# Optimization experiments

Hardware: AMD Instinct MI355X
Metric: run time of the kernel (lower is better)

Reference implementation:

```python
import jax, jax.numpy as jnp
import numpy as np


def _conv2d(x, w, b, dilation=1):
    pad = dilation * (w.shape[-1] // 2)
    y = jax.lax.conv_general_dilated(x, w, (1, 1), [(pad, pad), (pad, pad)],
                                     rhs_dilation=(dilation, dilation),
                                     dimension_numbers=("NCHW", "OIHW", "NCHW"))
    return y + b[None, :, None, None]


def _bn(x, gamma, beta, mean, var):
    # eval-mode BatchNorm2d, eps=1e-5
    inv = gamma / jnp.sqrt(var + 1e-5)
    return (x - mean[None, :, None, None]) * inv[None, :, None, None] + beta[None, :, None, None]


def _frft2d(x, angles):
    # Faithful port of the source frft2d, including the quirk that
    # temp[shft, :] indexes the BATCH dim: since shft is a permutation of
    # 0..N-1, the net effect is that batch entries 0..N-1 get (i)fft'd along
    # axis -2 and entries >= N are untouched.
    temp = jnp.swapaxes(x, -1, -2)
    BC = temp.shape[0]
    for a in angles:
        a = a % 4
        N = temp.shape[-2]
        sN = np.float32(np.sqrt(N))
        mask = (jnp.arange(BC) < N)[:, None, None]
        if a == 1:
            temp = jnp.where(mask, jnp.fft.fft(temp, axis=-2) / sN, temp)
        elif a == 2:
            temp = jnp.flip(temp, axis=-2)
        elif a == 3:
            temp = jnp.where(mask, jnp.fft.ifft(temp, axis=-2) * sN, temp)
        temp = jnp.swapaxes(temp, -1, -2)
    return temp


def setup_inputs() -> dict:
    key = jax.random.key(0)
    ks = jax.random.split(key, 12)
    B, C, H, W = 4, 64, 256, 256
    f = lambda k, shape, s=0.1: jax.random.normal(k, shape, dtype=jnp.float32) * s
    z1 = jnp.zeros((1,), jnp.float32)
    o1 = jnp.ones((1,), jnp.float32)
    return {
        "x": jax.random.normal(ks[0], (B, C, H, W), dtype=jnp.float32),
        "kernel_map": jnp.ones((H, W), dtype=jnp.float32),
        "theta_w": f(ks[1], (1, 1, 3, 3)), "theta_b": z1,
        "phase_w": f(ks[2], (1, 1, 3, 3)), "phase_b": z1,
        "phase_gamma": o1, "phase_beta": z1, "phase_mean": z1, "phase_var": o1,
        "amp_w": f(ks[3], (1, 1, 1, 1)), "amp_b": z1,
        "ms_w1": f(ks[4], (1, 1, 3, 3)), "ms_b1": z1,
        "ms_w2": f(ks[5], (1, 1, 3, 3)), "ms_b2": z1,
        "ms_w3": f(ks[6], (1, 1, 3, 3)), "ms_b3": z1,
        "fc1_w": f(ks[7], (16, 1)), "fc1_b": jnp.zeros((16,), jnp.float32),
        "fc2_w": f(ks[8], (1, 16)), "fc2_b": z1,
        "fin_w": f(ks[9], (1, 6, 1, 1)), "fin_b": z1,
        "fin_gamma": o1, "fin_beta": z1, "fin_mean": z1, "fin_var": o1,
    }


def reference(x, kernel_map, theta_w, theta_b, phase_w, phase_b,
              phase_gamma, phase_beta, phase_mean, phase_var,
              amp_w, amp_b, ms_w1, ms_b1, ms_w2, ms_b2, ms_w3, ms_b3,
              fc1_w, fc1_b, fc2_w, fc2_b, fin_w, fin_b,
              fin_gamma, fin_beta, fin_mean, fin_var):
    B, C, H, W = x.shape
    BC = B * C
    xf = x.reshape(BC, H, W)
    trker = jnp.clip(jax.nn.softplus(kernel_map), 1e-3, 10.0)
    # Riesz kernels, p=(1,1) => sin(pi/2)
    Y = (jnp.arange(H, dtype=jnp.float32) + 1.0)[:, None]
    X = (jnp.arange(W, dtype=jnp.float32) + 1.0)[None, :]
    sa = np.float32(np.sin(0.5 * np.pi))
    denom = jnp.sqrt((X / sa) ** 2 + (Y / sa) ** 2) + 1e-6
    dx = ((-1j) * (X / sa) / denom).astype(jnp.complex64) * trker
    dy = ((-1j) * (Y / sa) / denom).astype(jnp.complex64) * trker
    fa = _frft2d(xf.astype(jnp.complex64), [1, 1])
    R1 = jnp.abs(_frft2d(dx * fa, [-1, -1])) + 1e-6
    R2 = jnp.abs(_frft2d(dy * fa, [-1, -1])) + 1e-6
    A = jnp.sqrt(jax.nn.relu(xf ** 2 + R1 ** 2 + R2 ** 2) + 1e-6)[:, None]
    P = jnp.arctan2(jnp.sqrt(R1 ** 2 + R2 ** 2) + 1e-6, xf + 1e-6)[:, None]
    theta = jnp.arctan2(R2, R1 + 1e-6)[:, None]
    G_theta = theta * jax.nn.sigmoid(_conv2d(theta, theta_w, theta_b))
    P_prime = jax.nn.relu(_bn(_conv2d(P, phase_w, phase_b),
                              phase_gamma, phase_beta, phase_mean, phase_var))
    A_boost = A + jax.nn.relu(_conv2d(A, amp_w, amp_b))
    ms = jnp.concatenate([_conv2d(A_boost, ms_w1, ms_b1, 1),
                          _conv2d(A_boost, ms_w2, ms_b2, 2),
                          _conv2d(A_boost, ms_w3, ms_b3, 3)], axis=1)
    # adaptive_avg_pool2d to (H, W) is the identity here
    gf = jnp.mean(A_boost, axis=(2, 3))  # (BC, 1)
    gw = jax.nn.sigmoid(jax.nn.relu(gf @ fc1_w.T + fc1_b) @ fc2_w.T + fc2_b)
    gw = gw[:, :, None, None]  # (BC,1,1,1)
    fusion = jnp.concatenate([A_boost, P_prime, G_theta, ms * gw], axis=1)  # (BC,6,H,W)
    fused = _bn(_conv2d(fusion, fin_w, fin_b), fin_gamma, fin_beta, fin_mean, fin_var)
    fused = jnp.clip(jax.nn.relu(fused), 0.0, 1.0)
    return fused.reshape(B, C, H, W)
```

## Files before the change

### kernel.cpp

```cpp
#include <hip/hip_runtime.h>
#include <hip/hip_fp16.h>
#include <math.h>

#define PI_F 3.14159265358979323846f
#define ROWB 2112ull
#define IMGB (ROWB * 256ull)

__device__ __forceinline__ unsigned rev8(unsigned v){ return __brev(v) >> 24; }

__device__ __forceinline__ float2 cmulf(float2 a, float2 b){ return make_float2(a.x*b.x - a.y*b.y, a.x*b.y + a.y*b.x); }
__device__ __forceinline__ float2 cmulc(float2 a, float2 b){ return make_float2(a.x*b.x + a.y*b.y, a.y*b.x - a.x*b.y); }
__device__ __forceinline__ float2 cadd (float2 a, float2 b){ return make_float2(a.x+b.x, a.y+b.y); }
__device__ __forceinline__ float2 csub (float2 a, float2 b){ return make_float2(a.x-b.x, a.y-b.y); }
__device__ __forceinline__ float2 eix(float a){ float s, c; __sincosf(a, &s, &c); return make_float2(c, s); }
__device__ __forceinline__ float2 sx(float2 v, int d){ return make_float2(__shfl_xor(v.x, d), __shfl_xor(v.y, d)); }

__device__ __forceinline__ float frcp(float x){ float r; asm("v_rcp_f32 %0, %1" : "=v"(r) : "v"(x)); return r; }

__device__ __forceinline__ float fast_atan2pos(float y, float x){
  const float ax = fabsf(x);
  const float mn = fminf(ax, y), mx = fmaxf(ax, y);
  const float t  = mn * frcp(mx);
  const float z  = t * t;
  float p = -0.01172120f;
  p = fmaf(p, z,  0.05265332f);
  p = fmaf(p, z, -0.11643287f);
  p = fmaf(p, z,  0.19354346f);
  p = fmaf(p, z, -0.33262347f);
  p = fmaf(p, z,  0.99997726f);
  p = p * t;
  p = (y > ax) ? (1.57079632679f - p) : p;
  p = (x < 0.f) ? (3.14159265359f - p) : p;
  return p;
}

__device__ __forceinline__ unsigned packh2u(float a, float b){
  return __builtin_bit_cast(unsigned, __floats2half2_rn(a, b));
}
__device__ __forceinline__ float2 unpackh2(float p){
  return __half22float2(__builtin_bit_cast(__half2, p));
}

struct Twid { float2 w, w2, t[6]; };
__device__ __forceinline__ void mktw(Twid& T, int lane){
  T.w  = eix(-(2.0f * PI_F / 256.0f) * (float)lane);
  T.w2 = cmulf(T.w, T.w);
  #pragma unroll
  for (int st = 0; st < 6; ++st){
    const int d = 32 >> st;
    T.t[st] = eix(-(PI_F / (float)d) * (float)(lane & (d - 1)));
  }
}

__device__ __forceinline__ void fft256_fwd(float2 v[4], int lane, const Twid& T){
  const float2 t0 = cadd(v[0], v[2]);
  const float2 b0 = cmulf(csub(v[0], v[2]), T.w);
  const float2 t1 = cadd(v[1], v[3]);
  const float2 w64 = make_float2(T.w.y, -T.w.x);
  const float2 b1 = cmulf(csub(v[1], v[3]), w64);
  v[0] = cadd(t0, t1);
  v[1] = cmulf(csub(t0, t1), T.w2);
  v[2] = cadd(b0, b1);
  v[3] = cmulf(csub(b0, b1), T.w2);
  #pragma unroll
  for (int st = 0; st < 6; ++st){
    const int d = 32 >> st;
    const float2 tw = T.t[st];
    const bool hi = (lane & d) != 0;
    #pragma unroll
    for (int s = 0; s < 4; ++s){
      const float2 p  = sx(v[s], d);
      const float2 bo = cmulf(csub(p, v[s]), tw);
      const float2 lo = cadd(v[s], p);
      v[s] = hi ? bo : lo;
    }
  }
}

__device__ __forceinline__ void fft256_inv(float2 v[4], int lane, const Twid& T){
  #pragma unroll
  for (int st = 0; st < 6; ++st){
    const int d = 1 << st;
    const float2 tw = T.t[5 - st];
    const bool hi = (lane & d) != 0;
    #pragma unroll
    for (int s = 0; s < 4; ++s){
      const float2 p = sx(v[s], d);
      const float2 m = cmulc(hi ? v[s] : p, tw);
      v[s] = hi ? csub(p, m) : cadd(v[s], m);
    }
  }
  const float2 m1 = cmulc(v[1], T.w2);
  const float2 m3a = cmulc(v[3], T.w2);
  const float2 n0 = cadd(v[0], m1), n1 = csub(v[0], m1);
  const float2 n2 = cadd(v[2], m3a), n3 = csub(v[2], m3a);
  const float2 m2 = cmulc(n2, T.w);
  const float2 uci = make_float2(T.w.y, T.w.x);
  const float2 m3 = cmulf(n3, uci);
  v[0] = cadd(n0, m2); v[2] = csub(n0, m2);
  v[1] = cadd(n1, m3); v[3] = csub(n1, m3);
}

__global__ __launch_bounds__(256) void k0_prep(const float* __restrict__ km,
                                               float* __restrict__ sTabS,
                                               float* __restrict__ zrow){
  const int idx = blockIdx.x * 256 + threadIdx.x;
  const int q = idx >> 8, r = idx & 255;
  const int u = rev8(q), v = rev8(r);
  const float kv = km[u * 256 + v];
  float sp = fmaxf(kv, 0.f) + log1pf(expf(-fabsf(kv)));
  sp = fminf(fmaxf(sp, 1e-3f), 10.f);
  const float fu = (float)(u + 1), fv = (float)(v + 1);
  sTabS[idx] = sp / (sqrtf(fu * fu + fv * fv) + 1e-6f) * (1.0f / 65536.0f);
  if (blockIdx.x == 0){
    zrow[threadIdx.x] = 0.f;
    zrow[threadIdx.x + 256] = 0.f;
    if (threadIdx.x < 16) zrow[threadIdx.x + 512] = 0.f;
  }
}

__global__ __launch_bounds__(256) void k1_row(const float* __restrict__ x, char* __restrict__ arena){
  const int grp = threadIdx.x >> 6, lane = threadIdx.x & 63;
  const int rs = blockIdx.x * 4 + grp;
  Twid T; mktw(T, lane);
  const float* xr = x + (size_t)rs * 256;
  float2 v[4];
  #pragma unroll
  for (int s = 0; s < 4; ++s) v[s] = make_float2(xr[lane + 64 * s], 0.f);
  fft256_fwd(v, lane, T);
  float2* S = (float2*)(arena + (size_t)rs * ROWB);
  #pragma unroll
  for (int s = 0; s < 4; ++s) S[lane + 64 * s] = v[s];
}

__global__ __launch_bounds__(256) void k2_col(char* __restrict__ arena, const float* __restrict__ sTabS){
  __shared__ float2 lds[256 * 9];
  const int tid = threadIdx.x;
  const int b  = blockIdx.x >> 5;
  const int u0 = (blockIdx.x & 31) << 3;
  char* base = arena + (size_t)b * IMGB;

  #pragma unroll
  for (int k = 0; k < 8; ++k){
    const int idx = tid + (k << 8);
    const int r = idx >> 3, cc = idx & 7;
    lds[r * 9 + (cc ^ ((r >> 3) & 7))] = *(const float2*)(base + (size_t)r * ROWB + (size_t)(u0 + cc) * 8);
  }
  __syncthreads();

  const int wv = tid >> 6, lane = tid & 63;
  Twid T; mktw(T, lane);
  const int r6 = __brev(lane) >> 26;
  float fvv[4];
  fvv[0] = (float)(4 * r6 + 0 + 1);
  fvv[1] = (float)(4 * r6 + 2 + 1);
  fvv[2] = (float)(4 * r6 + 1 + 1);
  fvv[3] = (float)(4 * r6 + 3 + 1);
  const int swb = (lane >> 3) & 7;

  uint2 res0[4], res1[4];
  #pragma unroll
  for (int cp = 0; cp < 2; ++cp){
    const int c = wv * 2 + cp;
    const int q = u0 + c;
    const int swc = c ^ swb;
    float2 F[4];
    #pragma unroll
    for (int s = 0; s < 4; ++s) F[s] = lds[(lane + 64 * s) * 9 + swc];
    fft256_fwd(F, lane, T);
    float sc[4];
    #pragma unroll
    for (int s = 0; s < 4; ++s) sc[s] = sTabS[q * 256 + lane + 64 * s];
    const float fu = (float)(rev8((unsigned)q) + 1);
    float2 G[4];
    #pragma unroll
    for (int s = 0; s < 4; ++s){ const float a = fvv[s] * sc[s]; G[s] = make_float2(a * F[s].y, -a * F[s].x); }
    fft256_inv(G, lane, T);
    #pragma unroll
    for (int s = 0; s < 4; ++s){ (cp ? res1 : res0)[s].x = packh2u(G[s].x, G[s].y); }
    #pragma unroll
    for (int s = 0; s < 4; ++s){ const float a = fu * sc[s]; G[s] = make_float2(a * F[s].y, -a * F[s].x); }
    fft256_inv(G, lane, T);
    #pragma unroll
    for (int s = 0; s < 4; ++s){ (cp ? res1 : res0)[s].y = packh2u(G[s].x, G[s].y); }
  }
  __syncthreads();
  #pragma unroll
  for (int cp = 0; cp < 2; ++cp){
    const int c = wv * 2 + cp;
    const int swc = c ^ swb;
    #pragma unroll
    for (int s = 0; s < 4; ++s){
      const uint2 rr = cp ? res1[s] : res0[s];
      lds[(lane + 64 * s) * 9 + swc] = make_float2(__uint_as_float(rr.x), __uint_as_float(rr.y));
    }
  }
  __syncthreads();
  #pragma unroll
  for (int k = 0; k < 8; ++k){
    const int idx = tid + (k << 8);
    const int r = idx >> 3, cc = idx & 7;
    *(float2*)(base + (size_t)r * ROWB + (size_t)(u0 + cc) * 8) = lds[r * 9 + (cc ^ ((r >> 3) & 7))];
  }
}

__global__ __launch_bounds__(256) void k3_rowinv(const float* __restrict__ x, char* __restrict__ arena,
    const float* __restrict__ ampw, const float* __restrict__ ampb,
    float* __restrict__ rowsum){
  const int grp = threadIdx.x >> 6, lane = threadIdx.x & 63;
  const int rs = blockIdx.x * 4 + grp;
  Twid T; mktw(T, lane);
  char* rowb = arena + (size_t)rs * ROWB;
  float2 g1[4], g2[4];
  #pragma unroll
  for (int s = 0; s < 4; ++s){
    const float2 pk = *(const float2*)(rowb + (size_t)(lane + 64 * s) * 8);
    g1[s] = unpackh2(pk.x); g2[s] = unpackh2(pk.y);
  }
  fft256_inv(g1, lane, T);
  fft256_inv(g2, lane, T);
  const float aw = *ampw, ab = *ampb;
  const float* xr = x + (size_t)rs * 256;
  float* Arow = (float*)(rowb + 16);
  unsigned* Prow = (unsigned*)(rowb + 1072);
  float sum = 0.f;
  #pragma unroll
  for (int s = 0; s < 4; ++s){
    const int j = lane + 64 * s;
    const float xv = xr[j];
    const float R1 = sqrtf(fmaf(g1[s].x, g1[s].x, g1[s].y * g1[s].y)) + 1e-6f;
    const float R2 = sqrtf(fmaf(g2[s].x, g2[s].x, g2[s].y * g2[s].y)) + 1e-6f;
    const float rr = fmaf(R1, R1, R2 * R2);
    const float A = sqrtf(fmaxf(fmaf(xv, xv, rr), 0.f) + 1e-6f);
    const float P  = fast_atan2pos(sqrtf(rr) + 1e-6f, xv + 1e-6f);
    const float Th = fast_atan2pos(R2, R1 + 1e-6f);
    const float Ab = A + fmaxf(fmaf(aw, A, ab), 0.f);
    Arow[j] = Ab;
    Prow[j] = packh2u(P, Th);
    sum += Ab;
  }
  #pragma unroll
  for (int off = 32; off; off >>= 1) sum += __shfl_down(sum, off);
  if (lane == 0) rowsum[rs] = sum;
}

__global__ __launch_bounds__(256) void kpad(char* __restrict__ arena){
  char* row = arena + (size_t)blockIdx.x * IMGB + (size_t)threadIdx.x * ROWB;
  const float4 z = make_float4(0.f, 0.f, 0.f, 0.f);
  *(float4*)(row)         = z;
  *(float4*)(row + 1040)  = z;
  *(float4*)(row + 1056)  = z;
  *(float4*)(row + 2096)  = z;
}

__global__ __launch_bounds__(256) void k4_gw(const float* __restrict__ rowsum,
    const float* __restrict__ fc1w, const float* __restrict__ fc1b,
    const float* __restrict__ fc2w, const float* __restrict__ fc2b,
    float* __restrict__ gw){
  __shared__ float red[256];
  const int tid = threadIdx.x;
  red[tid] = rowsum[blockIdx.x * 256 + tid];
  __syncthreads();
  #pragma unroll
  for (int off = 128; off; off >>= 1){
    if (tid < off) red[tid] += red[tid + off];
    __syncthreads();
  }
  if (tid == 0){
    const float gf = red[0] * (1.0f / 65536.0f);
    float acc = fc2b[0];
    #pragma unroll
    for (int k = 0; k < 16; ++k)
      acc += fc2w[k] * fmaxf(gf * fc1w[k] + fc1b[k], 0.f);
    gw[blockIdx.x] = frcp(1.f + __expf(-acc));
  }
}

__global__ __launch_bounds__(256) void k5_fuse(
    const char* __restrict__ arena, const float* __restrict__ zrowf,
    const float* __restrict__ gwp,
    const float* __restrict__ theta_w, const float* __restrict__ theta_b,
    const float* __restrict__ phase_w, const float* __restrict__ phase_b,
    const float* __restrict__ phase_gamma, const float* __restrict__ phase_beta,
    const float* __restrict__ phase_mean, const float* __restrict__ phase_var,
    const float* __restrict__ ms_w1, const float* __restrict__ ms_b1,
    const float* __restrict__ ms_w2, const float* __restrict__ ms_b2,
    const float* __restrict__ ms_w3, const float* __restrict__ ms_b3,
    const float* __restrict__ fin_w, const float* __restrict__ fin_b,
    const float* __restrict__ fin_gamma, const float* __restrict__ fin_beta,
    const float* __restrict__ fin_mean, const float* __restrict__ fin_var,
    float* __restrict__ out){
  const int z = blockIdx.z;
  const int tx = threadIdx.x & 15, ty = threadIdx.x >> 4;
  const int j0 = (blockIdx.x << 6) + (tx << 2);
  const int i0 = (blockIdx.y << 6) + (ty << 2);
  const char* img = arena + (size_t)z * IMGB;

  float tw9[9], pw9[9], w1[9], w2[9], w3[9];
  #pragma unroll
  for (int k = 0; k < 9; ++k){
    tw9[k] = theta_w[k]; pw9[k] = phase_w[k];
    w1[k] = ms_w1[k]; w2[k] = ms_w2[k]; w3[k] = ms_w3[k];
  }
  const float b1s = ms_b1[0], b2s = ms_b2[0], b3s = ms_b3[0];
  const float tbs = theta_b[0], pbs = phase_b[0];

  float4 m1[4], m2[4], m3[4], at[4], ap[4], Ac[4], Tc[4];
  #pragma unroll
  for (int oi = 0; oi < 4; ++oi){
    m1[oi] = make_float4(b1s, b1s, b1s, b1s);
    m2[oi] = make_float4(b2s, b2s, b2s, b2s);
    m3[oi] = make_float4(b3s, b3s, b3s, b3s);
    at[oi] = make_float4(tbs, tbs, tbs, tbs);
    ap[oi] = make_float4(pbs, pbs, pbs, pbs);
  }

  #pragma unroll
  for (int lr = 0; lr < 10; ++lr){
    const int ar = i0 - 3 + lr;
    const float* rowA = ((unsigned)ar < 256u) ? (const float*)(img + (size_t)ar * ROWB) : zrowf;
    const float4 va = *(const float4*)(rowA + j0);
    const float4 vb = *(const float4*)(rowA + j0 + 4);
    const float4 vc = *(const float4*)(rowA + j0 + 8);
    const float a[12] = {va.x, va.y, va.z, va.w, vb.x, vb.y, vb.z, vb.w, vc.x, vc.y, vc.z, vc.w};
    #pragma unroll
    for (int oi = 0; oi < 4; ++oi){
      const int dd = lr - 3 - oi;
      if (dd >= -1 && dd <= 1){
        const int wr = (dd + 1) * 3;
        #pragma unroll
        for (int dx = -1; dx <= 1; ++dx){
          const float w = w1[wr + dx + 1];
          m1[oi].x += w * a[4 + 0 + dx]; m1[oi].y += w * a[4 + 1 + dx];
          m1[oi].z += w * a[4 + 2 + dx]; m1[oi].w += w * a[4 + 3 + dx];
        }
      }
      if (dd == -2 || dd == 0 || dd == 2){
        const int wr = (dd / 2 + 1) * 3;
        #pragma unroll
        for (int dx = -1; dx <= 1; ++dx){
          const float w = w2[wr + dx + 1];
          m2[oi].x += w * a[4 + 0 + 2 * dx]; m2[oi].y += w * a[4 + 1 + 2 * dx];
          m2[oi].z += w * a[4 + 2 + 2 * dx]; m2[oi].w += w * a[4 + 3 + 2 * dx];
        }
      }
      if (dd == -3 || dd == 0 || dd == 3){
        const int wr = (dd / 3 + 1) * 3;
        #pragma unroll
        for (int dx = -1; dx <= 1; ++dx){
          const float w = w3[wr + dx + 1];
          m3[oi].x += w * a[4 + 0 + 3 * dx]; m3[oi].y += w * a[4 + 1 + 3 * dx];
          m3[oi].z += w * a[4 + 2 + 3 * dx]; m3[oi].w += w * a[4 + 3 + 3 * dx];
        }
      }
      if (dd == 0) Ac[oi] = make_float4(a[4], a[5], a[6], a[7]);
    }
  }

  #pragma unroll
  for (int lr = 0; lr < 6; ++lr){
    const int ar = i0 - 1 + lr;
    const unsigned* rowP = ((unsigned)ar < 256u) ? (const unsigned*)(img + (size_t)ar * ROWB + 1056)
                                                 : (const unsigned*)zrowf;
    const uint4 ua = *(const uint4*)(rowP + j0);
    const uint4 ub = *(const uint4*)(rowP + j0 + 4);
    const uint4 uc = *(const uint4*)(rowP + j0 + 8);
    const unsigned uu[12] = {ua.x, ua.y, ua.z, ua.w, ub.x, ub.y, ub.z, ub.w, uc.x, uc.y, uc.z, uc.w};
    float p[12], t[12];
    #pragma unroll
    for (int k = 0; k < 12; ++k){
      const float2 pt = unpackh2(__builtin_bit_cast(float, uu[k]));
      p[k] = pt.x; t[k] = pt.y;
    }
    #pragma unroll
    for (int oi = 0; oi < 4; ++oi){
      const int dd = lr - 1 - oi;
      if (dd >= -1 && dd <= 1){
        const int wr = (dd + 1) * 3;
        #pragma unroll
        for (int dx = -1; dx <= 1; ++dx){
          const float wp = pw9[wr + dx + 1], wt = tw9[wr + dx + 1];
          ap[oi].x += wp * p[4 + 0 + dx]; ap[oi].y += wp * p[4 + 1 + dx];
          ap[oi].z += wp * p[4 + 2 + dx]; ap[oi].w += wp * p[4 + 3 + dx];
          at[oi].x += wt * t[4 + 0 + dx]; at[oi].y += wt * t[4 + 1 + dx];
          at[oi].z += wt * t[4 + 2 + dx]; at[oi].w += wt * t[4 + 3 + dx];
        }
      }
      if (dd == 0) Tc[oi] = make_float4(t[4], t[5], t[6], t[7]);
    }
  }

  const float gwb = gwp[z];
  const float inv_p = phase_gamma[0] * rsqrtf(phase_var[0] + 1e-5f);
  const float pmean = phase_mean[0], pbeta = phase_beta[0];
  const float f0 = fin_w[0], f1 = fin_w[1], f2 = fin_w[2];
  const float f3 = fin_w[3], f4 = fin_w[4], f5 = fin_w[5];
  const float fb = fin_b[0];
  const float inv_f = fin_gamma[0] * rsqrtf(fin_var[0] + 1e-5f);
  const float fmean = fin_mean[0], fbeta = fin_beta[0];

  #pragma unroll
  for (int oi = 0; oi < 4; ++oi){
    const float mm1[4] = {m1[oi].x, m1[oi].y, m1[oi].z, m1[oi].w};
    const float mm2[4] = {m2[oi].x, m2[oi].y, m2[oi].z, m2[oi].w};
    const float mm3[4] = {m3[oi].x, m3[oi].y, m3[oi].z, m3[oi].w};
    const float tt[4]  = {at[oi].x, at[oi].y, at[oi].z, at[oi].w};
    const float pp[4]  = {ap[oi].x, ap[oi].y, ap[oi].z, ap[oi].w};
    const float ac[4]  = {Ac[oi].x, Ac[oi].y, Ac[oi].z, Ac[oi].w};
    const float tc[4]  = {Tc[oi].x, Tc[oi].y, Tc[oi].z, Tc[oi].w};
    float o4[4];
    #pragma unroll
    for (int oj = 0; oj < 4; ++oj){
      const float Gt = tc[oj] * frcp(1.f + __expf(-tt[oj]));
      const float Pp = fmaxf((pp[oj] - pmean) * inv_p + pbeta, 0.f);
      const float pre = f0 * ac[oj] + f1 * Pp + f2 * Gt
                      + gwb * (f3 * mm1[oj] + f4 * mm2[oj] + f5 * mm3[oj]) + fb;
      float o = (pre - fmean) * inv_f + fbeta;
      o4[oj] = fminf(fmaxf(o, 0.f), 1.f);
    }
    *(float4*)(out + ((size_t)(z * 256 + i0 + oi) << 8) + j0) = make_float4(o4[0], o4[1], o4[2], o4[3]);
  }
}

extern "C" void kernel_launch(void* const* d_in, const int* in_sizes, int n_in,
                              void* d_out, int out_size, void* d_ws, size_t ws_size,
                              hipStream_t stream){
  const float* x  = (const float*)d_in[0];
  const float* km = (const float*)d_in[1];

  int N = 1;
  while (N < 64){
    const size_t need = (size_t)(256 / N) * IMGB + 2112ull + 262144ull + 1024ull
                      + (size_t)(256 / N) * 1024ull;
    if (need <= ws_size) break;
    N <<= 1;
  }
  const int imgsPer = 256 / N;
  const int rowsPer = imgsPer * 256;

  char*  ws     = (char*)d_ws;
  char*  arena  = ws;
  float* zrow   = (float*)(ws + (size_t)imgsPer * IMGB);
  float* sTabS  = (float*)(ws + (size_t)imgsPer * IMGB + 2112ull);
  float* gwbuf  = (float*)(ws + (size_t)imgsPer * IMGB + 2112ull + 262144ull);
  float* rowsum = (float*)(ws + (size_t)imgsPer * IMGB + 2112ull + 262144ull + 1024ull);

  k0_prep<<<256, 256, 0, stream>>>(km, sTabS, zrow);

  for (int s = 0; s < N; ++s){
    const float* xs = x + (size_t)s * rowsPer * 256;
    float* outs = (float*)d_out + (size_t)s * rowsPer * 256;

    k1_row<<<rowsPer / 4, 256, 0, stream>>>(xs, arena);
    k2_col<<<imgsPer * 32, 256, 0, stream>>>(arena, sTabS);
    k3_rowinv<<<rowsPer / 4, 256, 0, stream>>>(xs, arena,
        (const float*)d_in[10], (const float*)d_in[11], rowsum);
    kpad<<<imgsPer, 256, 0, stream>>>(arena);
    k4_gw<<<imgsPer, 256, 0, stream>>>(rowsum,
        (const float*)d_in[18], (const float*)d_in[19],
        (const float*)d_in[20], (const float*)d_in[21], gwbuf);
    k5_fuse<<<dim3(4, 4, imgsPer), 256, 0, stream>>>(
        arena, zrow, gwbuf,
        (const float*)d_in[2],  (const float*)d_in[3],
        (const float*)d_in[4],  (const float*)d_in[5],
        (const float*)d_in[6],  (const float*)d_in[7],
        (const float*)d_in[8],  (const float*)d_in[9],
        (const float*)d_in[12], (const float*)d_in[13],
        (const float*)d_in[14], (const float*)d_in[15],
        (const float*)d_in[16], (const float*)d_in[17],
        (const float*)d_in[22], (const float*)d_in[23],
        (const float*)d_in[24], (const float*)d_in[25],
        (const float*)d_in[26], (const float*)d_in[27],
        outs);
  }
}
```

Measured before the change: 376.9 us.

## Widen column-FFT tiles, write results in place, and branchless FFT butterflies

The radix-2 butterfly stages in the forward and inverse 256-point FFTs become a branchless linear combination, v*A + p*B, with per-lane coefficients chosen once per stage. This replaces the select between two computed results. The column kernel now handles 16 columns per block instead of 8, using a doubled LDS buffer, so it launches half as many blocks. Each wave writes its results straight back into its LDS slot rather than holding them in registers, which drops one barrier. The change trades fewer, larger blocks (more LDS per block, possibly lower occupancy) for wider coalesced row segments and less sync overhead.

```diff
diff --git a/kernel.cpp b/kernel.cpp
--- a/kernel.cpp
+++ b/kernel.cpp
@@ -52,6 +52,13 @@
   }
 }
 
+__device__ __forceinline__ float2 stage_ab(float2 v, float2 p, float Ax, float Ay, float Bx, float By){
+  float2 o;
+  o.x = v.x*Ax - v.y*Ay + p.x*Bx - p.y*By;
+  o.y = v.x*Ay + v.y*Ax + p.x*By + p.y*Bx;
+  return o;
+}
+
 __device__ __forceinline__ void fft256_fwd(float2 v[4], int lane, const Twid& T){
   const float2 t0 = cadd(v[0], v[2]);
   const float2 b0 = cmulf(csub(v[0], v[2]), T.w);
@@ -65,14 +72,14 @@
   #pragma unroll
   for (int st = 0; st < 6; ++st){
     const int d = 32 >> st;
-    const float2 tw = T.t[st];
+    const float2 t = T.t[st];
     const bool hi = (lane & d) != 0;
+    const float Ax = hi ? -t.x : 1.f, Ay = hi ? -t.y : 0.f;
+    const float Bx = hi ?  t.x : 1.f, By = hi ?  t.y : 0.f;
     #pragma unroll
     for (int s = 0; s < 4; ++s){
-      const float2 p  = sx(v[s], d);
-      const float2 bo = cmulf(csub(p, v[s]), tw);
-      const float2 lo = cadd(v[s], p);
-      v[s] = hi ? bo : lo;
+      const float2 p = sx(v[s], d);
+      v[s] = stage_ab(v[s], p, Ax, Ay, Bx, By);
     }
   }
 }
@@ -81,13 +88,14 @@
   #pragma unroll
   for (int st = 0; st < 6; ++st){
     const int d = 1 << st;
-    const float2 tw = T.t[5 - st];
+    const float2 t = T.t[5 - st];
     const bool hi = (lane & d) != 0;
+    const float Ax = hi ? -t.x : 1.f, Ay = hi ?  t.y : 0.f;
+    const float Bx = hi ?  1.f : t.x, By = hi ?  0.f : -t.y;
     #pragma unroll
     for (int s = 0; s < 4; ++s){
       const float2 p = sx(v[s], d);
-      const float2 m = cmulc(hi ? v[s] : p, tw);
-      v[s] = hi ? csub(p, m) : cadd(v[s], m);
+      v[s] = stage_ab(v[s], p, Ax, Ay, Bx, By);
     }
   }
   const float2 m1 = cmulc(v[1], T.w2);
@@ -134,17 +142,18 @@
 }
 
 __global__ __launch_bounds__(256) void k2_col(char* __restrict__ arena, const float* __restrict__ sTabS){
-  __shared__ float2 lds[256 * 9];
+  __shared__ float2 lds[2][256 * 9];
   const int tid = threadIdx.x;
-  const int b  = blockIdx.x >> 5;
-  const int u0 = (blockIdx.x & 31) << 3;
+  const int b  = blockIdx.x >> 4;
+  const int u0 = (blockIdx.x & 15) << 4;
   char* base = arena + (size_t)b * IMGB;
 
   #pragma unroll
-  for (int k = 0; k < 8; ++k){
+  for (int k = 0; k < 16; ++k){
     const int idx = tid + (k << 8);
-    const int r = idx >> 3, cc = idx & 7;
-    lds[r * 9 + (cc ^ ((r >> 3) & 7))] = *(const float2*)(base + (size_t)r * ROWB + (size_t)(u0 + cc) * 8);
+    const int r = idx >> 4, cc = idx & 15;
+    lds[cc >> 3][r * 9 + ((cc & 7) ^ ((r >> 3) & 7))] =
+        *(const float2*)(base + (size_t)r * ROWB + (size_t)(u0 + cc) * 8);
   }
   __syncthreads();
 
@@ -158,15 +167,15 @@
   fvv[3] = (float)(4 * r6 + 3 + 1);
   const int swb = (lane >> 3) & 7;
 
-  uint2 res0[4], res1[4];
-  #pragma unroll
-  for (int cp = 0; cp < 2; ++cp){
-    const int c = wv * 2 + cp;
+  #pragma unroll
+  for (int cp = 0; cp < 4; ++cp){
+    const int c = wv * 4 + cp;
     const int q = u0 + c;
-    const int swc = c ^ swb;
+    float2* buf = lds[c >> 3];
+    const int swc = (c & 7) ^ swb;
     float2 F[4];
     #pragma unroll
-    for (int s = 0; s < 4; ++s) F[s] = lds[(lane + 64 * s) * 9 + swc];
+    for (int s = 0; s < 4; ++s) F[s] = buf[(lane + 64 * s) * 9 + swc];
     fft256_fwd(F, lane, T);
     float sc[4];
     #pragma unroll
@@ -176,31 +185,24 @@
     #pragma unroll
     for (int s = 0; s < 4; ++s){ const float a = fvv[s] * sc[s]; G[s] = make_float2(a * F[s].y, -a * F[s].x); }
     fft256_inv(G, lane, T);
-    #pragma unroll
-    for (int s = 0; s < 4; ++s){ (cp ? res1 : res0)[s].x = packh2u(G[s].x, G[s].y); }
+    unsigned u1h[4];
+    #pragma unroll
+    for (int s = 0; s < 4; ++s) u1h[s] = packh2u(G[s].x, G[s].y);
     #pragma unroll
     for (int s = 0; s < 4; ++s){ const float a = fu * sc[s]; G[s] = make_float2(a * F[s].y, -a * F[s].x); }
     fft256_inv(G, lane, T);
     #pragma unroll
-    for (int s = 0; s < 4; ++s){ (cp ? res1 : res0)[s].y = packh2u(G[s].x, G[s].y); }
+    for (int s = 0; s < 4; ++s)
+      buf[(lane + 64 * s) * 9 + swc] =
+          make_float2(__uint_as_float(u1h[s]), __uint_as_float(packh2u(G[s].x, G[s].y)));
   }
   __syncthreads();
   #pragma unroll
-  for (int cp = 0; cp < 2; ++cp){
-    const int c = wv * 2 + cp;
-    const int swc = c ^ swb;
-    #pragma unroll
-    for (int s = 0; s < 4; ++s){
-      const uint2 rr = cp ? res1[s] : res0[s];
-      lds[(lane + 64 * s) * 9 + swc] = make_float2(__uint_as_float(rr.x), __uint_as_float(rr.y));
-    }
-  }
-  __syncthreads();
-  #pragma unroll
-  for (int k = 0; k < 8; ++k){
+  for (int k = 0; k < 16; ++k){
     const int idx = tid + (k << 8);
-    const int r = idx >> 3, cc = idx & 7;
-    *(float2*)(base + (size_t)r * ROWB + (size_t)(u0 + cc) * 8) = lds[r * 9 + (cc ^ ((r >> 3) & 7))];
+    const int r = idx >> 4, cc = idx & 15;
+    *(float2*)(base + (size_t)r * ROWB + (size_t)(u0 + cc) * 8) =
+        lds[cc >> 3][r * 9 + ((cc & 7) ^ ((r >> 3) & 7))];
   }
 }
 
@@ -452,7 +454,7 @@
     float* outs = (float*)d_out + (size_t)s * rowsPer * 256;
 
     k1_row<<<rowsPer / 4, 256, 0, stream>>>(xs, arena);
-    k2_col<<<imgsPer * 32, 256, 0, stream>>>(arena, sTabS);
+    k2_col<<<imgsPer * 16, 256, 0, stream>>>(arena, sTabS);
     k3_rowinv<<<rowsPer / 4, 256, 0, stream>>>(xs, arena,
         (const float*)d_in[10], (const float*)d_in[11], rowsum);
     kpad<<<imgsPer, 256, 0, stream>>>(arena);
```

Measured after the change: 405.1 us. 7.5% more time.
